# Kernel optimization log

Hardware: AMD Instinct MI355X
Metric: run time of the kernel (lower is better)

## Reference

```python
import jax, jax.numpy as jnp
from jax import lax
import numpy as np

EPS = 1e-5


def setup_inputs() -> dict:
    key = jax.random.key(0)
    ks = jax.random.split(key, 16)
    N, C, H, W = 8, 128, 128, 128
    MIP, OUP, K = 8, 128, 3
    inp = {}
    inp["x"] = jax.random.normal(ks[0], (N, C, H, W), dtype=jnp.float32)
    # conv1: 1x1, C -> MIP
    inp["w1"] = jax.random.normal(ks[1], (MIP, C), dtype=jnp.float32) * (1.0 / np.sqrt(C))
    inp["b1"] = jax.random.normal(ks[2], (MIP,), dtype=jnp.float32) * 0.02
    # bn1 (inference: frozen running stats)
    inp["g1"] = jnp.ones((MIP,), jnp.float32) + jax.random.normal(ks[3], (MIP,), jnp.float32) * 0.02
    inp["be1"] = jax.random.normal(ks[4], (MIP,), jnp.float32) * 0.02
    inp["m1"] = jax.random.normal(ks[5], (MIP,), jnp.float32) * 0.02
    inp["v1"] = jnp.ones((MIP,), jnp.float32)
    # conv_h / conv_w: 1x1, MIP -> C
    inp["wh"] = jax.random.normal(ks[6], (C, MIP), dtype=jnp.float32) * (1.0 / np.sqrt(MIP))
    inp["bh"] = jax.random.normal(ks[7], (C,), dtype=jnp.float32) * 0.02
    inp["ww"] = jax.random.normal(ks[8], (C, MIP), dtype=jnp.float32) * (1.0 / np.sqrt(MIP))
    inp["bw"] = jax.random.normal(ks[9], (C,), dtype=jnp.float32) * 0.02
    # final conv: KxK, C -> OUP
    inp["wc"] = jax.random.normal(ks[10], (OUP, C, K, K), dtype=jnp.float32) * (1.0 / np.sqrt(C * K * K))
    inp["bc"] = jax.random.normal(ks[11], (OUP,), dtype=jnp.float32) * 0.02
    inp["g2"] = jnp.ones((OUP,), jnp.float32) + jax.random.normal(ks[12], (OUP,), jnp.float32) * 0.02
    inp["be2"] = jax.random.normal(ks[13], (OUP,), jnp.float32) * 0.02
    inp["m2"] = jax.random.normal(ks[14], (OUP,), jnp.float32) * 0.02
    inp["v2"] = jnp.ones((OUP,), jnp.float32)
    return inp


def _bn1d(y, g, b, m, v):
    # y: (n, c, l); per-channel affine with frozen stats
    s = g / jnp.sqrt(v + EPS)
    return y * s[None, :, None] + (b - m * s)[None, :, None]


def _h_swish(y):
    return y * jnp.clip(y + 3.0, 0.0, 6.0) / 6.0


def reference(x, w1, b1, g1, be1, m1, v1, wh, bh, ww, bw, wc, bc, g2, be2, m2, v2):
    n, c, h, w = x.shape
    # Multi-scale pooled descriptors. Nearest interp of the 2-bin and 4-bin
    # adaptive pools back to length-1 picks bin 0, i.e. the mean over the
    # first half / first quarter of the pooled axis.
    x_h = x.mean(3) + x[..., : w // 2].mean(3) + x[..., : w // 4].mean(3)        # (n,c,h)
    x_w = x.mean(2) + x[:, :, : h // 2].mean(2) + x[:, :, : h // 4].mean(2)      # (n,c,w)
    y = jnp.concatenate([x_h, x_w], axis=2)                                       # (n,c,h+w)
    y = jnp.einsum('ncl,mc->nml', y, w1) + b1[None, :, None]                      # 1x1 conv
    y = _h_swish(_bn1d(y, g1, be1, m1, v1))
    xh, xw = y[:, :, :h], y[:, :, h:]
    a_h = jax.nn.sigmoid(jnp.einsum('nml,cm->ncl', xh, wh) + bh[None, :, None])[:, :, :, None]  # (n,c,h,1)
    a_w = jax.nn.sigmoid(jnp.einsum('nml,cm->ncl', xw, ww) + bw[None, :, None])[:, :, None, :]  # (n,c,1,w)
    out = x * a_w * a_h                                                           # gated features
    # final conv (kernel 3, stride 1, pad 1) + BN + SiLU
    out = lax.conv_general_dilated(out, wc, window_strides=(1, 1),
                                   padding=[(1, 1), (1, 1)],
                                   dimension_numbers=('NCHW', 'OIHW', 'NCHW'))
    out = out + bc[None, :, None, None]
    s2 = g2 / jnp.sqrt(v2 + EPS)
    out = out * s2[None, :, None, None] + (be2 - m2 * s2)[None, :, None, None]
    return out * jax.nn.sigmoid(out)
```

## Files before the change

### kernel.cpp

```cpp
#include <hip/hip_runtime.h>
#include <hip/hip_bf16.h>

typedef float f32x4 __attribute__((ext_vector_type(4)));
typedef __bf16 bf16x8 __attribute__((ext_vector_type(8)));

#define EPSF 1e-5f

__device__ __forceinline__ float pw(int i) {
    return (1.0f + (i < 64 ? 2.0f : 0.0f) + (i < 32 ? 4.0f : 0.0f)) * (1.0f / 128.0f);
}

__global__ __launch_bounds__(256) void pool_kernel(const float* __restrict__ x,
                                                   float* __restrict__ P) {
    int nc = blockIdx.x;
    const f32x4* plane = (const f32x4*)(x + (size_t)nc * 16384);
    __shared__ float rowpart[128][33];
    __shared__ __align__(16) f32x4 colpart[8][32];
    int t = threadIdx.x;
    int wq = t & 31, hg = t >> 5;
    f32x4 cacc = {0.f, 0.f, 0.f, 0.f};
    float u0 = pw(wq * 4), u1 = pw(wq * 4 + 1), u2 = pw(wq * 4 + 2), u3 = pw(wq * 4 + 3);
    #pragma unroll
    for (int j = 0; j < 16; ++j) {
        int r = hg * 16 + j;
        f32x4 v = plane[r * 32 + wq];
        rowpart[r][wq] = v.x * u0 + v.y * u1 + v.z * u2 + v.w * u3;
        cacc += v * pw(r);
    }
    colpart[hg][wq] = cacc;
    __syncthreads();
    float s = 0.f;
    if (t < 128) {
        #pragma unroll
        for (int q = 0; q < 32; ++q) s += rowpart[t][q];
        P[(size_t)nc * 256 + t] = s;
    } else {
        int w = t - 128;
        const float* cp = (const float*)colpart;
        #pragma unroll
        for (int g = 0; g < 8; ++g) s += cp[g * 128 + w];
        P[(size_t)nc * 256 + 128 + w] = s;
    }
}

__global__ __launch_bounds__(256) void attn_wtrans_kernel(const float* __restrict__ P,
    const float* __restrict__ w1, const float* __restrict__ b1,
    const float* __restrict__ g1, const float* __restrict__ be1,
    const float* __restrict__ m1, const float* __restrict__ v1,
    const float* __restrict__ wh, const float* __restrict__ bh,
    const float* __restrict__ ww, const float* __restrict__ bw,
    const float* __restrict__ wc, const float* __restrict__ bc,
    const float* __restrict__ g2, const float* __restrict__ be2,
    const float* __restrict__ m2, const float* __restrict__ v2,
    float* __restrict__ A2, __hip_bfloat16* __restrict__ Wt, float* __restrict__ ab) {
    int t = threadIdx.x;
    if (blockIdx.x >= 32) {
        int g = (blockIdx.x - 32) * 256 + t;
        int step = g >> 12, rem = g & 4095;
        int o = rem >> 5, m = rem & 31;
        int slotp = m >> 3, j = m & 7;
        int u = slotp ^ ((o >> 1) & 3);
        int kidx = u * 8 + j;
        int khw = step >> 2, c32 = step & 3;
        int c = c32 * 32 + kidx;
        Wt[g] = __float2bfloat16(wc[(o * 128 + c) * 9 + khw]);
        if (g < 128) {
            float s2 = g2[g] * rsqrtf(v2[g] + EPSF);
            ab[g] = s2;
            ab[128 + g] = bc[g] * s2 + be2[g] - m2[g] * s2;
        }
        return;
    }
    int n = blockIdx.x >> 2, cg = blockIdx.x & 3;
    __shared__ float w1s[1024], whs[256], wws[256];
    __shared__ float bhs[32], bws[32];
    __shared__ float s1[8], t1[8], b1s[8];
    for (int i = t; i < 1024; i += 256) w1s[i] = w1[i];
    whs[t] = wh[cg * 256 + t];
    wws[t] = ww[cg * 256 + t];
    if (t < 32) { bhs[t] = bh[cg * 32 + t]; bws[t] = bw[cg * 32 + t]; }
    if (t < 8) {
        float s = g1[t] * rsqrtf(v1[t] + EPSF);
        s1[t] = s; t1[t] = be1[t] - m1[t] * s; b1s[t] = b1[t];
    }
    __syncthreads();
    float y[8];
    #pragma unroll
    for (int m = 0; m < 8; ++m) y[m] = b1s[m];
    const float* Pn = P + (size_t)n * 32768;
    for (int c = 0; c < 128; ++c) {
        float pv = Pn[c * 256 + t];
        #pragma unroll
        for (int m = 0; m < 8; ++m) y[m] += w1s[m * 128 + c] * pv;
    }
    #pragma unroll
    for (int m = 0; m < 8; ++m) {
        float v = y[m] * s1[m] + t1[m];
        float cl = fminf(fmaxf(v + 3.f, 0.f), 6.f);
        y[m] = v * cl * (1.f / 6.f);
    }
    const float* Ws_ = (t < 128) ? whs : wws;
    const float* Bs = (t < 128) ? bhs : bws;
    float* On = A2 + (size_t)n * 32768;
    for (int cc = 0; cc < 32; ++cc) {
        int c = cg * 32 + cc;
        float a = Bs[cc];
        #pragma unroll
        for (int m = 0; m < 8; ++m) a += y[m] * Ws_[cc * 8 + m];
        On[c * 256 + t] = 1.f / (1.f + __expf(-a));
    }
}

__device__ __forceinline__ int ldsoff(int w, int c) {
    return w * 128 + ((((c >> 3) ^ ((w & 7) << 1)) << 3) | (c & 7));
}

__global__ __launch_bounds__(256) void amul_kernel(const float* __restrict__ x,
    const float* __restrict__ A2, __hip_bfloat16* __restrict__ Xpad) {
    int nh = blockIdx.x;
    int n = nh >> 7, h = nh & 127;
    int t = threadIdx.x;
    __shared__ __align__(16) __hip_bfloat16 T[16384];
    __shared__ float ahs[128];
    if (t < 128) ahs[t] = A2[(size_t)(n * 128 + t) * 256 + h];

    uint4 z = {0u, 0u, 0u, 0u};
    __hip_bfloat16* Xn = Xpad + (size_t)n * 16900 * 128;
    if (t < 32) {
        int wp = (t & 1) ? 129 : 0, cb2 = t >> 1;
        *(uint4*)(Xn + (size_t)((h + 1) * 130 + wp) * 128 + cb2 * 8) = z;
    }
    if (h == 0 || h == 127) {
        int hp = (h == 0) ? 0 : 129;
        for (int i = t; i < 2080; i += 256) {
            int wp = i >> 4, cb2 = i & 15;
            *(uint4*)(Xn + (size_t)(hp * 130 + wp) * 128 + cb2 * 8) = z;
        }
    }
    __syncthreads();

    const float* xr  = x + ((size_t)n * 128 * 128 + h) * 128;
    const float* awr = A2 + (size_t)n * 32768 + 128;
    #pragma unroll
    for (int j = 0; j < 16; ++j) {
        int item = j * 256 + t;
        int c = item >> 5, w4 = item & 31;
        f32x4 xv = *(const f32x4*)(xr + (size_t)c * 16384 + w4 * 4);
        f32x4 av = *(const f32x4*)(awr + c * 256 + w4 * 4);
        float ah = ahs[c];
        #pragma unroll
        for (int k = 0; k < 4; ++k) {
            float val = xv[k] * av[k] * ah;
            T[ldsoff(w4 * 4 + k, c)] = __float2bfloat16(val);
        }
    }
    __syncthreads();
    __hip_bfloat16* orow = Xn + (size_t)((h + 1) * 130 + 1) * 128;
    #pragma unroll
    for (int j = 0; j < 8; ++j) {
        int item = j * 256 + t;
        int w = item >> 4, cb = item & 15;
        int slot = cb ^ ((w & 7) << 1);
        uint4 v = *(const uint4*)&T[w * 128 + slot * 8];
        *(uint4*)(orow + w * 128 + cb * 8) = v;
    }
}

__global__ __launch_bounds__(512, 4) void conv_kernel(
    const __hip_bfloat16* __restrict__ Xpad, const __hip_bfloat16* __restrict__ Wt,
    const float* __restrict__ ab, float* __restrict__ out) {
    int bid = blockIdx.x;
    int work = (bid & 7) * 64 + (bid >> 3);
    int n = work >> 6, h0 = (work & 63) * 2;
    int tid = threadIdx.x;
    int lane = tid & 63, wid = tid >> 6;
    int wm = wid >> 2, wn = wid & 3;
    int r16 = lane & 15, u = lane >> 4;

    __shared__ __align__(16) __hip_bfloat16 Ws[3 * 4096];
    __shared__ __align__(16) __hip_bfloat16 Xs[3 * 8192];

    const __hip_bfloat16* Xn = Xpad + ((size_t)n * 16900 + (size_t)h0 * 130) * 128;

    int offA[4], offB[4];
    #pragma unroll
    for (int mi = 0; mi < 4; ++mi) {
        int o = wm * 64 + mi * 16 + r16;
        offA[mi] = o * 32 + ((u ^ ((o >> 1) & 3)) << 3);
    }
    #pragma unroll
    for (int ni = 0; ni < 4; ++ni) {
        int p = wn * 64 + ni * 16 + r16;
        offB[ni] = p * 32 + ((u ^ ((p >> 1) & 3)) << 3);
    }

    int xo[2];
    #pragma unroll
    for (int j = 0; j < 2; ++j) {
        int idx = j * 512 + tid, p = idx >> 2, s = idx & 3;
        int r2 = p >> 7, w = p & 127;
        xo[j] = (r2 * 130 + w) * 128 + ((s ^ ((p >> 1) & 3)) << 3);
    }

    auto stage = [&](int t) {
        int khw = t >> 2, c32 = t & 3;
        int kh = khw / 3, kw = khw - kh * 3;
        __builtin_amdgcn_global_load_lds(
            (const __attribute__((address_space(1))) void*)(Wt + t * 4096 + tid * 8),
            (__attribute__((address_space(3))) void*)(&Ws[(t % 3) * 4096 + tid * 8]),
            16, 0, 0);
        const __hip_bfloat16* xsrc = Xn + (kh * 130 + kw) * 128 + c32 * 32;
        __hip_bfloat16* xdst = &Xs[(t % 3) * 8192];
        #pragma unroll
        for (int j = 0; j < 2; ++j)
            __builtin_amdgcn_global_load_lds(
                (const __attribute__((address_space(1))) void*)(xsrc + xo[j]),
                (__attribute__((address_space(3))) void*)(xdst + (j * 512 + tid) * 8),
                16, 0, 0);
    };

    f32x4 acc[4][4];
    #pragma unroll
    for (int i = 0; i < 4; ++i)
        #pragma unroll
        for (int j = 0; j < 4; ++j) acc[i][j] = (f32x4){0.f, 0.f, 0.f, 0.f};

    stage(0);
    stage(1);
    asm volatile("s_waitcnt vmcnt(3)" ::: "memory");
    __builtin_amdgcn_sched_barrier(0);
    __builtin_amdgcn_s_barrier();
    __builtin_amdgcn_sched_barrier(0);

    #pragma unroll
    for (int t = 0; t < 36; ++t) {
        const __hip_bfloat16* Wb = &Ws[(t % 3) * 4096];
        const __hip_bfloat16* Xr = &Xs[(t % 3) * 8192];
        if (t + 2 < 36) stage(t + 2);

        bf16x8 fa[4], fb[4];
        #pragma unroll
        for (int mi = 0; mi < 4; ++mi) fa[mi] = *(const bf16x8*)&Wb[offA[mi]];
        #pragma unroll
        for (int ni = 0; ni < 4; ++ni) fb[ni] = *(const bf16x8*)&Xr[offB[ni]];
        #pragma unroll
        for (int mi = 0; mi < 4; ++mi)
            #pragma unroll
            for (int ni = 0; ni < 4; ++ni)
                acc[mi][ni] = __builtin_amdgcn_mfma_f32_16x16x32_bf16(
                    fa[mi], fb[ni], acc[mi][ni], 0, 0, 0);

        if (t < 34) {
            asm volatile("s_waitcnt vmcnt(3)" ::: "memory");
        } else if (t == 34) {
            asm volatile("s_waitcnt vmcnt(0)" ::: "memory");
        }
        __builtin_amdgcn_sched_barrier(0);
        if (t < 35) {
            __builtin_amdgcn_s_barrier();
            __builtin_amdgcn_sched_barrier(0);
        }
    }

    #pragma unroll
    for (int mi = 0; mi < 4; ++mi) {
        #pragma unroll
        for (int r = 0; r < 4; ++r) {
            int o = wm * 64 + mi * 16 + u * 4 + r;
            float al = ab[o], be = ab[128 + o];
            size_t obase = (((size_t)n * 128 + o) * 128 + h0) * 128;
            #pragma unroll
            for (int ni = 0; ni < 4; ++ni) {
                int p = wn * 64 + ni * 16 + r16;
                int r2 = p >> 7, w = p & 127;
                float z = acc[mi][ni][r] * al + be;
                out[obase + r2 * 128 + w] = z / (1.f + __expf(-z));
            }
        }
    }
}

extern "C" void kernel_launch(void* const* d_in, const int* in_sizes, int n_in,
                              void* d_out, int out_size, void* d_ws, size_t ws_size,
                              hipStream_t stream) {
    const float* x   = (const float*)d_in[0];
    const float* w1  = (const float*)d_in[1];
    const float* b1  = (const float*)d_in[2];
    const float* g1  = (const float*)d_in[3];
    const float* be1 = (const float*)d_in[4];
    const float* m1  = (const float*)d_in[5];
    const float* v1  = (const float*)d_in[6];
    const float* wh  = (const float*)d_in[7];
    const float* bh  = (const float*)d_in[8];
    const float* ww  = (const float*)d_in[9];
    const float* bw  = (const float*)d_in[10];
    const float* wc  = (const float*)d_in[11];
    const float* bc  = (const float*)d_in[12];
    const float* g2  = (const float*)d_in[13];
    const float* be2 = (const float*)d_in[14];
    const float* m2  = (const float*)d_in[15];
    const float* v2  = (const float*)d_in[16];
    float* out = (float*)d_out;

    char* ws = (char*)d_ws;
    float* P  = (float*)(ws);
    float* A2 = (float*)(ws + (1 << 20));
    __hip_bfloat16* Xpad = (__hip_bfloat16*)(ws + (2 << 20));
    __hip_bfloat16* Wt   = (__hip_bfloat16*)(ws + (2 << 20) + 34611200);
    float* ab = (float*)(ws + (2 << 20) + 34611200 + 294912);

    pool_kernel<<<1024, 256, 0, stream>>>(x, P);
    attn_wtrans_kernel<<<608, 256, 0, stream>>>(P, w1, b1, g1, be1, m1, v1,
                                                wh, bh, ww, bw, wc, bc, g2, be2, m2, v2,
                                                A2, Wt, ab);
    amul_kernel<<<1024, 256, 0, stream>>>(x, A2, Xpad);
    conv_kernel<<<512, 512, 0, stream>>>(Xpad, Wt, ab, out);
}
```

Measured before the change: 108.1 us.

## Double conv tile to four output rows and split stage into two MFMA phases

The conv kernel now handles four output rows per block instead of two. That doubles the X tile held in LDS and gives 128 accumulators per thread, which halves the grid to 256 blocks and improves reuse of each weight tile. Each K-step is split into two half-phases that interleave LDS fragment loads, async global-to-LDS prefetch and MFMA groups, separated by extra barriers and s_setprio hints. The cost is higher register and LDS use, lower occupancy (launch bounds drop to 2 waves per SIMD), and only 256 blocks to fill the machine.

Result: slower. 113.4 us (+4.9%).

```diff
diff --git a/kernel.cpp b/kernel.cpp
--- a/kernel.cpp
+++ b/kernel.cpp
@@ -166,68 +166,70 @@
     }
 }
 
-__global__ __launch_bounds__(512, 4) void conv_kernel(
+__global__ __launch_bounds__(512, 2) void conv_kernel(
     const __hip_bfloat16* __restrict__ Xpad, const __hip_bfloat16* __restrict__ Wt,
     const float* __restrict__ ab, float* __restrict__ out) {
     int bid = blockIdx.x;
-    int work = (bid & 7) * 64 + (bid >> 3);
-    int n = work >> 6, h0 = (work & 63) * 2;
+    int work = (bid & 7) * 32 + (bid >> 3);
+    int n = work >> 5, h0 = (work & 31) * 4;
     int tid = threadIdx.x;
     int lane = tid & 63, wid = tid >> 6;
     int wm = wid >> 2, wn = wid & 3;
     int r16 = lane & 15, u = lane >> 4;
 
     __shared__ __align__(16) __hip_bfloat16 Ws[3 * 4096];
-    __shared__ __align__(16) __hip_bfloat16 Xs[3 * 8192];
+    __shared__ __align__(16) __hip_bfloat16 Xs[3 * 16384];
 
     const __hip_bfloat16* Xn = Xpad + ((size_t)n * 16900 + (size_t)h0 * 130) * 128;
 
-    int offA[4], offB[4];
+    int offA[4], offB[8];
     #pragma unroll
     for (int mi = 0; mi < 4; ++mi) {
         int o = wm * 64 + mi * 16 + r16;
         offA[mi] = o * 32 + ((u ^ ((o >> 1) & 3)) << 3);
     }
     #pragma unroll
-    for (int ni = 0; ni < 4; ++ni) {
-        int p = wn * 64 + ni * 16 + r16;
+    for (int ni = 0; ni < 8; ++ni) {
+        int p = wn * 128 + ni * 16 + r16;
         offB[ni] = p * 32 + ((u ^ ((p >> 1) & 3)) << 3);
     }
 
-    int xo[2];
-    #pragma unroll
-    for (int j = 0; j < 2; ++j) {
+    int xo[4];
+    #pragma unroll
+    for (int j = 0; j < 4; ++j) {
         int idx = j * 512 + tid, p = idx >> 2, s = idx & 3;
         int r2 = p >> 7, w = p & 127;
         xo[j] = (r2 * 130 + w) * 128 + ((s ^ ((p >> 1) & 3)) << 3);
     }
 
-    auto stage = [&](int t) {
-        int khw = t >> 2, c32 = t & 3;
-        int kh = khw / 3, kw = khw - kh * 3;
+    auto stageW = [&](int t) {
         __builtin_amdgcn_global_load_lds(
             (const __attribute__((address_space(1))) void*)(Wt + t * 4096 + tid * 8),
             (__attribute__((address_space(3))) void*)(&Ws[(t % 3) * 4096 + tid * 8]),
             16, 0, 0);
+    };
+    auto stageX = [&](int t, int jlo, int jhi) {
+        int khw = t >> 2, c32 = t & 3;
+        int kh = khw / 3, kw = khw - kh * 3;
         const __hip_bfloat16* xsrc = Xn + (kh * 130 + kw) * 128 + c32 * 32;
-        __hip_bfloat16* xdst = &Xs[(t % 3) * 8192];
-        #pragma unroll
-        for (int j = 0; j < 2; ++j)
+        __hip_bfloat16* xdst = &Xs[(t % 3) * 16384];
+        #pragma unroll
+        for (int j = jlo; j < jhi; ++j)
             __builtin_amdgcn_global_load_lds(
                 (const __attribute__((address_space(1))) void*)(xsrc + xo[j]),
                 (__attribute__((address_space(3))) void*)(xdst + (j * 512 + tid) * 8),
                 16, 0, 0);
     };
 
-    f32x4 acc[4][4];
+    f32x4 acc[4][8];
     #pragma unroll
     for (int i = 0; i < 4; ++i)
         #pragma unroll
-        for (int j = 0; j < 4; ++j) acc[i][j] = (f32x4){0.f, 0.f, 0.f, 0.f};
-
-    stage(0);
-    stage(1);
-    asm volatile("s_waitcnt vmcnt(3)" ::: "memory");
+        for (int j = 0; j < 8; ++j) acc[i][j] = (f32x4){0.f, 0.f, 0.f, 0.f};
+
+    stageW(0); stageX(0, 0, 4);
+    stageW(1); stageX(1, 0, 4);
+    asm volatile("s_waitcnt vmcnt(5)" ::: "memory");
     __builtin_amdgcn_sched_barrier(0);
     __builtin_amdgcn_s_barrier();
     __builtin_amdgcn_sched_barrier(0);
@@ -235,23 +237,46 @@
     #pragma unroll
     for (int t = 0; t < 36; ++t) {
         const __hip_bfloat16* Wb = &Ws[(t % 3) * 4096];
-        const __hip_bfloat16* Xr = &Xs[(t % 3) * 8192];
-        if (t + 2 < 36) stage(t + 2);
+        const __hip_bfloat16* Xr = &Xs[(t % 3) * 16384];
+        bool pre = (t + 2 < 36);
 
         bf16x8 fa[4], fb[4];
         #pragma unroll
         for (int mi = 0; mi < 4; ++mi) fa[mi] = *(const bf16x8*)&Wb[offA[mi]];
         #pragma unroll
         for (int ni = 0; ni < 4; ++ni) fb[ni] = *(const bf16x8*)&Xr[offB[ni]];
+        if (pre) { stageW(t + 2); stageX(t + 2, 0, 2); }
+        __builtin_amdgcn_s_barrier();
+        asm volatile("s_waitcnt lgkmcnt(0)" ::: "memory");
+        __builtin_amdgcn_sched_barrier(0);
+        __builtin_amdgcn_s_setprio(1);
         #pragma unroll
         for (int mi = 0; mi < 4; ++mi)
             #pragma unroll
             for (int ni = 0; ni < 4; ++ni)
                 acc[mi][ni] = __builtin_amdgcn_mfma_f32_16x16x32_bf16(
                     fa[mi], fb[ni], acc[mi][ni], 0, 0, 0);
+        __builtin_amdgcn_s_setprio(0);
+        __builtin_amdgcn_s_barrier();
+
+        bf16x8 fc[4];
+        #pragma unroll
+        for (int ni = 0; ni < 4; ++ni) fc[ni] = *(const bf16x8*)&Xr[offB[4 + ni]];
+        if (pre) stageX(t + 2, 2, 4);
+        __builtin_amdgcn_s_barrier();
+        asm volatile("s_waitcnt lgkmcnt(0)" ::: "memory");
+        __builtin_amdgcn_sched_barrier(0);
+        __builtin_amdgcn_s_setprio(1);
+        #pragma unroll
+        for (int mi = 0; mi < 4; ++mi)
+            #pragma unroll
+            for (int ni = 0; ni < 4; ++ni)
+                acc[mi][4 + ni] = __builtin_amdgcn_mfma_f32_16x16x32_bf16(
+                    fa[mi], fc[ni], acc[mi][4 + ni], 0, 0, 0);
+        __builtin_amdgcn_s_setprio(0);
 
         if (t < 34) {
-            asm volatile("s_waitcnt vmcnt(3)" ::: "memory");
+            asm volatile("s_waitcnt vmcnt(5)" ::: "memory");
         } else if (t == 34) {
             asm volatile("s_waitcnt vmcnt(0)" ::: "memory");
         }
@@ -270,8 +295,8 @@
             float al = ab[o], be = ab[128 + o];
             size_t obase = (((size_t)n * 128 + o) * 128 + h0) * 128;
             #pragma unroll
-            for (int ni = 0; ni < 4; ++ni) {
-                int p = wn * 64 + ni * 16 + r16;
+            for (int ni = 0; ni < 8; ++ni) {
+                int p = wn * 128 + ni * 16 + r16;
                 int r2 = p >> 7, w = p & 127;
                 float z = acc[mi][ni][r] * al + be;
                 out[obase + r2 * 128 + w] = z / (1.f + __expf(-z));
@@ -314,5 +339,5 @@
                                                 wh, bh, ww, bw, wc, bc, g2, be2, m2, v2,
                                                 A2, Wt, ab);
     amul_kernel<<<1024, 256, 0, stream>>>(x, A2, Xpad);
-    conv_kernel<<<512, 512, 0, stream>>>(Xpad, Wt, ab, out);
-}
+    conv_kernel<<<256, 512, 0, stream>>>(Xpad, Wt, ab, out);
+}
```

## Split pooling per half-plane and move weight transform into pool kernel

Applied to the files above, without the earlier changes.

The pooling kernel now launches two blocks per (n,c) plane, each reducing half the rows. Column partial sums are written to a separate buffer and combined later in the attention kernel. The conv weight transpose/bf16 conversion is moved from the attention kernel into the pooling launch, so the small 32-block attention kernel no longer carries that extra work. This doubles pooling parallelism and shortens the serial attention stage, at the cost of an extra partial-sum buffer and an extra read and add during attention.

Result: no change. 109.3 us (+1.1%).

```diff
diff --git a/kernel.cpp b/kernel.cpp
--- a/kernel.cpp
+++ b/kernel.cpp
@@ -10,52 +10,15 @@
     return (1.0f + (i < 64 ? 2.0f : 0.0f) + (i < 32 ? 4.0f : 0.0f)) * (1.0f / 128.0f);
 }
 
-__global__ __launch_bounds__(256) void pool_kernel(const float* __restrict__ x,
-                                                   float* __restrict__ P) {
-    int nc = blockIdx.x;
-    const f32x4* plane = (const f32x4*)(x + (size_t)nc * 16384);
-    __shared__ float rowpart[128][33];
-    __shared__ __align__(16) f32x4 colpart[8][32];
-    int t = threadIdx.x;
-    int wq = t & 31, hg = t >> 5;
-    f32x4 cacc = {0.f, 0.f, 0.f, 0.f};
-    float u0 = pw(wq * 4), u1 = pw(wq * 4 + 1), u2 = pw(wq * 4 + 2), u3 = pw(wq * 4 + 3);
-    #pragma unroll
-    for (int j = 0; j < 16; ++j) {
-        int r = hg * 16 + j;
-        f32x4 v = plane[r * 32 + wq];
-        rowpart[r][wq] = v.x * u0 + v.y * u1 + v.z * u2 + v.w * u3;
-        cacc += v * pw(r);
-    }
-    colpart[hg][wq] = cacc;
-    __syncthreads();
-    float s = 0.f;
-    if (t < 128) {
-        #pragma unroll
-        for (int q = 0; q < 32; ++q) s += rowpart[t][q];
-        P[(size_t)nc * 256 + t] = s;
-    } else {
-        int w = t - 128;
-        const float* cp = (const float*)colpart;
-        #pragma unroll
-        for (int g = 0; g < 8; ++g) s += cp[g * 128 + w];
-        P[(size_t)nc * 256 + 128 + w] = s;
-    }
-}
-
-__global__ __launch_bounds__(256) void attn_wtrans_kernel(const float* __restrict__ P,
-    const float* __restrict__ w1, const float* __restrict__ b1,
-    const float* __restrict__ g1, const float* __restrict__ be1,
-    const float* __restrict__ m1, const float* __restrict__ v1,
-    const float* __restrict__ wh, const float* __restrict__ bh,
-    const float* __restrict__ ww, const float* __restrict__ bw,
+__global__ __launch_bounds__(256) void pool_wtrans_kernel(const float* __restrict__ x,
     const float* __restrict__ wc, const float* __restrict__ bc,
     const float* __restrict__ g2, const float* __restrict__ be2,
     const float* __restrict__ m2, const float* __restrict__ v2,
-    float* __restrict__ A2, __hip_bfloat16* __restrict__ Wt, float* __restrict__ ab) {
+    float* __restrict__ P, float* __restrict__ Pc,
+    __hip_bfloat16* __restrict__ Wt, float* __restrict__ ab) {
     int t = threadIdx.x;
-    if (blockIdx.x >= 32) {
-        int g = (blockIdx.x - 32) * 256 + t;
+    if (blockIdx.x >= 2048) {
+        int g = (blockIdx.x - 2048) * 256 + t;
         int step = g >> 12, rem = g & 4095;
         int o = rem >> 5, m = rem & 31;
         int slotp = m >> 3, j = m & 7;
@@ -71,7 +34,48 @@
         }
         return;
     }
-    int n = blockIdx.x >> 2, cg = blockIdx.x & 3;
+    int b = blockIdx.x;
+    int nc = b >> 1, half = b & 1;
+    const f32x4* plane = (const f32x4*)(x + (size_t)nc * 16384 + half * 8192);
+    __shared__ float rowpart[64][33];
+    __shared__ __align__(16) f32x4 colpart[8][32];
+    int wq = t & 31, hg = t >> 5;
+    f32x4 cacc = {0.f, 0.f, 0.f, 0.f};
+    float u0 = pw(wq * 4), u1 = pw(wq * 4 + 1), u2 = pw(wq * 4 + 2), u3 = pw(wq * 4 + 3);
+    #pragma unroll
+    for (int j = 0; j < 8; ++j) {
+        int rl = hg * 8 + j;
+        int r = half * 64 + rl;
+        f32x4 v = plane[rl * 32 + wq];
+        rowpart[rl][wq] = v.x * u0 + v.y * u1 + v.z * u2 + v.w * u3;
+        cacc += v * pw(r);
+    }
+    colpart[hg][wq] = cacc;
+    __syncthreads();
+    if (t < 64) {
+        float s = 0.f;
+        #pragma unroll
+        for (int q = 0; q < 32; ++q) s += rowpart[t][q];
+        P[(size_t)nc * 256 + half * 64 + t] = s;
+    } else if (t >= 128) {
+        int w = t - 128;
+        const float* cp = (const float*)colpart;
+        float s = 0.f;
+        #pragma unroll
+        for (int g = 0; g < 8; ++g) s += cp[g * 128 + w];
+        Pc[(size_t)(half * 1024 + nc) * 128 + w] = s;
+    }
+}
+
+__global__ __launch_bounds__(256) void attn_kernel(const float* __restrict__ P,
+    const float* __restrict__ Pc,
+    const float* __restrict__ w1, const float* __restrict__ b1,
+    const float* __restrict__ g1, const float* __restrict__ be1,
+    const float* __restrict__ m1, const float* __restrict__ v1,
+    const float* __restrict__ wh, const float* __restrict__ bh,
+    const float* __restrict__ ww, const float* __restrict__ bw,
+    float* __restrict__ A2) {
+    int n = blockIdx.x >> 2, cg = blockIdx.x & 3, t = threadIdx.x;
     __shared__ float w1s[1024], whs[256], wws[256];
     __shared__ float bhs[32], bws[32];
     __shared__ float s1[8], t1[8], b1s[8];
@@ -87,11 +91,22 @@
     float y[8];
     #pragma unroll
     for (int m = 0; m < 8; ++m) y[m] = b1s[m];
-    const float* Pn = P + (size_t)n * 32768;
-    for (int c = 0; c < 128; ++c) {
-        float pv = Pn[c * 256 + t];
-        #pragma unroll
-        for (int m = 0; m < 8; ++m) y[m] += w1s[m * 128 + c] * pv;
+    const float* Pn  = P + (size_t)n * 32768;
+    const float* Pc0 = Pc + (size_t)n * 128 * 128;
+    const float* Pc1 = Pc0 + (size_t)1024 * 128;
+    if (t < 128) {
+        for (int c = 0; c < 128; ++c) {
+            float pv = Pn[c * 256 + t];
+            #pragma unroll
+            for (int m = 0; m < 8; ++m) y[m] += w1s[m * 128 + c] * pv;
+        }
+    } else {
+        int w = t - 128;
+        for (int c = 0; c < 128; ++c) {
+            float pv = Pc0[c * 128 + w] + Pc1[c * 128 + w];
+            #pragma unroll
+            for (int m = 0; m < 8; ++m) y[m] += w1s[m * 128 + c] * pv;
+        }
     }
     #pragma unroll
     for (int m = 0; m < 8; ++m) {
@@ -308,11 +323,12 @@
     __hip_bfloat16* Xpad = (__hip_bfloat16*)(ws + (2 << 20));
     __hip_bfloat16* Wt   = (__hip_bfloat16*)(ws + (2 << 20) + 34611200);
     float* ab = (float*)(ws + (2 << 20) + 34611200 + 294912);
-
-    pool_kernel<<<1024, 256, 0, stream>>>(x, P);
-    attn_wtrans_kernel<<<608, 256, 0, stream>>>(P, w1, b1, g1, be1, m1, v1,
-                                                wh, bh, ww, bw, wc, bc, g2, be2, m2, v2,
-                                                A2, Wt, ab);
+    float* Pc = (float*)(ws + (2 << 20) + 34611200 + 294912 + 4096);
+
+    pool_wtrans_kernel<<<2624, 256, 0, stream>>>(x, wc, bc, g2, be2, m2, v2,
+                                                 P, Pc, Wt, ab);
+    attn_kernel<<<32, 256, 0, stream>>>(P, Pc, w1, b1, g1, be1, m1, v1,
+                                        wh, bh, ww, bw, A2);
     amul_kernel<<<1024, 256, 0, stream>>>(x, A2, Xpad);
     conv_kernel<<<512, 512, 0, stream>>>(Xpad, Wt, ab, out);
 }
```
